# Performance work log

Measured on AMD Instinct MI355X. Metric: run time of the kernel, lower is better.

## Reference

```python
import jax, jax.numpy as jnp
import numpy as np

LR = 0.01
WD = 0.01


def _lfltm(params, x):
    w1, b1, w2, b2 = params
    return jnp.tanh(x @ w1 + b1) @ w2 + b2  # [N, D]


def _deep_opt_elem(Wm1, bm1, Wm2, bm2, g):
    # per-parameter-element learned optimizer: scalar grad -> hidden(M) -> scalar update
    h = jnp.tanh(g[..., None] * Wm1 + bm1)  # [..., M]
    return h @ Wm2 + bm2[0]


def setup_inputs() -> dict:
    key = jax.random.key(0)
    ks = jax.random.split(key, 8)
    N, D, H, M = 16384, 512, 1024, 32
    return {
        "x_t": jax.random.normal(ks[0], (N, D), jnp.float32),
        "x_target": jax.random.normal(ks[1], (N, D), jnp.float32),
        "w1": jax.random.normal(ks[2], (D, H), jnp.float32) * 0.02,
        "b1": jnp.zeros((H,), jnp.float32),
        "w2": jax.random.normal(ks[3], (H, D), jnp.float32) * 0.02,
        "b2": jnp.zeros((D,), jnp.float32),
        "Wm1": jax.random.normal(ks[4], (M,), jnp.float32) * 0.1,
        "bm1": jnp.zeros((M,), jnp.float32),
        "Wm2": jax.random.normal(ks[5], (M,), jnp.float32) * 0.1,
        "bm2": jnp.zeros((1,), jnp.float32),
    }


def reference(x_t, x_target, w1, b1, w2, b2, Wm1, bm1, Wm2, bm2):
    mem = (w1, b1, w2, b2)

    # retrieve: h_t = LFLTM(memory_state, x_t)
    h_t = _lfltm(mem, x_t)

    # analytic per-step gradient of MSE loss through the memory MLP
    def compute_loss(params):
        pred = _lfltm(params, x_t)
        return jnp.mean((pred - x_target) ** 2)

    grads = jax.grad(compute_loss)(mem)

    # learned optimizer on each gradient tensor, then fast-weight update
    new_mem = tuple(
        p - (LR * _deep_opt_elem(Wm1, bm1, Wm2, bm2, g) + WD * p)
        for p, g in zip(mem, grads)
    )

    return (h_t,) + new_mem
```

## Files before the change

kernel.cpp:

```cpp
#include <hip/hip_runtime.h>
#include <hip/hip_bf16.h>

#define LR 0.01f
#define WD 0.01f
#define NTHREADS 256
#define SCALE_G 1048576.0f
#define INV_SCALE_G 9.5367431640625e-07f

typedef short s16x8 __attribute__((ext_vector_type(8)));
typedef _Float16 f16x8 __attribute__((ext_vector_type(8)));
typedef float f32x4 __attribute__((ext_vector_type(4)));
typedef unsigned short u16;

__device__ __forceinline__ u16 f2h(float f) {
    _Float16 h = (_Float16)f;
    return *reinterpret_cast<u16*>(&h);
}
__device__ __forceinline__ float h2f(u16 u) {
    _Float16 h;
    *reinterpret_cast<u16*>(&h) = u;
    return (float)h;
}
__device__ __forceinline__ float tanh_fast(float x) {
    float t = fminf(fmaxf(2.f * x, -30.f), 30.f);
    float e = __expf(t);
    return 1.f - 2.f * __builtin_amdgcn_rcpf(e + 1.f);
}

__device__ __forceinline__ void stage_pair(const u16* gA, const u16* gB, int ldg,
                                           u16* lds) {
    const int t = threadIdx.x;
#pragma unroll
    for (int q = 0; q < 4; ++q) {
        int s = t + q * 256;
        int row = s >> 3, chp = s & 7;
        int chl = chp ^ (row & 7);
        const u16* gp = (chl < 4) ? (gA + (size_t)row * ldg + chl * 8)
                                  : (gB + (size_t)row * ldg + (chl & 3) * 8);
        __builtin_amdgcn_global_load_lds(
            (const __attribute__((address_space(1))) void*)gp,
            (__attribute__((address_space(3))) void*)(lds + s * 8), 16, 0, 0);
    }
}

__device__ __forceinline__ f16x8 frag(const u16* P, int r, int c) {
    return *(const f16x8*)(P + r * 64 + ((c ^ (r & 7)) * 8));
}

template <int EPI>
__global__ __launch_bounds__(NTHREADS) void k_mfma(
    const u16* __restrict__ A, const u16* __restrict__ Bt,
    int nbx, int Md, int Nd, int Kd, int Kslice,
    const float* __restrict__ bias, const float* __restrict__ xtgt,
    const u16* __restrict__ Th,
    float* __restrict__ outf, u16* __restrict__ outb, u16* __restrict__ outbT,
    float* __restrict__ gbias, float scale) {
    __shared__ u16 smem[2 * 8192];
    __shared__ float colacc[128];

    const int nwg = gridDim.x;
    const int sw = (blockIdx.x & 7) * (nwg >> 3) + (blockIdx.x >> 3);
    const int m0 = (sw / nbx) * 128, n0 = (sw % nbx) * 128;
    const int kb = blockIdx.y * Kslice;

    const int lane = threadIdx.x & 63, wid = threadIdx.x >> 6;
    const int wrow = (wid >> 1) * 64, wcol = (wid & 1) * 64;
    const int lm = lane & 15;
    const int cA = lane >> 4;

    f32x4 acc[4][4] = {};

    const u16* gA = A + (size_t)m0 * Kd + kb;
    const u16* gB = Bt + (size_t)n0 * Kd + kb;
    const int nt = Kslice >> 5;

    if (EPI == 1 || EPI == 2)
        if (threadIdx.x < 128) colacc[threadIdx.x] = 0.f;

    stage_pair(gA, gB, Kd, smem);
    stage_pair(gA + 32, gB + 32, Kd, smem + 8192);

    int cur = 0;
    for (int t = 0; t < nt; ++t, cur ^= 1) {
        if (t + 1 < nt) asm volatile("s_waitcnt vmcnt(4)" ::: "memory");
        else            asm volatile("s_waitcnt vmcnt(0)" ::: "memory");
        __builtin_amdgcn_s_barrier();

        const u16* P1 = smem + cur * 8192;
        f16x8 a[4], b[4];
#pragma unroll
        for (int i = 0; i < 4; ++i) {
            a[i] = frag(P1, wrow + i * 16 + lm, cA);
            b[i] = frag(P1, wcol + i * 16 + lm, cA + 4);
        }
        __builtin_amdgcn_s_setprio(1);
#pragma unroll
        for (int i = 0; i < 4; ++i)
#pragma unroll
            for (int j = 0; j < 4; ++j)
                acc[i][j] = __builtin_amdgcn_mfma_f32_16x16x32_f16(
                    a[i], b[j], acc[i][j], 0, 0, 0);
        __builtin_amdgcn_s_setprio(0);

        asm volatile("" ::: "memory");
        __builtin_amdgcn_s_barrier();
        if (t + 2 < nt)
            stage_pair(gA + (t + 2) * 32, gB + (t + 2) * 32, Kd,
                       smem + cur * 8192);
    }

    const int rbase = (lane >> 4) * 4;
#pragma unroll
    for (int i = 0; i < 4; ++i) {
        const int row0 = m0 + wrow + i * 16 + rbase;
#pragma unroll
        for (int j = 0; j < 4; ++j) {
            const int col = n0 + wcol + j * 16 + lm;
            if (EPI == 0) {
                ushort4 hv;
                float bcol = bias[col];
                hv.x = f2h(tanh_fast(acc[i][j][0] + bcol));
                hv.y = f2h(tanh_fast(acc[i][j][1] + bcol));
                hv.z = f2h(tanh_fast(acc[i][j][2] + bcol));
                hv.w = f2h(tanh_fast(acc[i][j][3] + bcol));
                outb[(size_t)(row0 + 0) * Nd + col] = hv.x;
                outb[(size_t)(row0 + 1) * Nd + col] = hv.y;
                outb[(size_t)(row0 + 2) * Nd + col] = hv.z;
                outb[(size_t)(row0 + 3) * Nd + col] = hv.w;
                *(ushort4*)(outbT + (size_t)col * Md + row0) = hv;
            } else if (EPI == 1) {
                ushort4 gv;
                float csum = 0.f;
#pragma unroll
                for (int r = 0; r < 4; ++r) {
                    size_t idx = (size_t)(row0 + r) * Nd + col;
                    float p = acc[i][j][r] + bias[col];
                    outf[idx] = p;
                    float gf = scale * (p - xtgt[idx]);
                    csum += gf;
                    u16 g = f2h(gf);
                    outb[idx] = g;
                    ((u16*)&gv)[r] = g;
                }
                *(ushort4*)(outbT + (size_t)col * Md + row0) = gv;
                atomicAdd(&colacc[wcol + j * 16 + lm], csum);
            } else if (EPI == 2) {
                ushort4 dv;
                float csum = 0.f;
#pragma unroll
                for (int r = 0; r < 4; ++r) {
                    size_t idx = (size_t)(row0 + r) * Nd + col;
                    float tv = h2f(Th[idx]);
                    float da = acc[i][j][r] * (1.0f - tv * tv);
                    csum += da;
                    ((u16*)&dv)[r] = f2h(da);
                }
                *(ushort4*)(outbT + (size_t)col * Md + row0) = dv;
                atomicAdd(&colacc[wcol + j * 16 + lm], csum);
            } else {
#pragma unroll
                for (int r = 0; r < 4; ++r)
                    atomicAdd(&outf[(size_t)(row0 + r) * Nd + col], acc[i][j][r]);
            }
        }
    }
    if (EPI == 1 || EPI == 2) {
        __syncthreads();
        if (threadIdx.x < 128)
            atomicAdd(&gbias[n0 + threadIdx.x], colacc[threadIdx.x]);
    }
}

__global__ void k_prep(const float* __restrict__ in, u16* __restrict__ rm,
                       u16* __restrict__ tr, int R, int C) {
    __shared__ float tile[64][65];
    const int tx = threadIdx.x & 63, ty = threadIdx.x >> 6;
    const int c0 = blockIdx.x * 64, r0 = blockIdx.y * 64;
#pragma unroll
    for (int i = 0; i < 64; i += 4) {
        size_t idx = (size_t)(r0 + ty + i) * C + c0 + tx;
        float v = in[idx];
        tile[ty + i][tx] = v;
        if (rm) rm[idx] = f2h(v);
    }
    __syncthreads();
    if (tr) {
#pragma unroll
        for (int i = 0; i < 64; i += 4)
            tr[(size_t)(c0 + ty + i) * R + r0 + tx] = f2h(tile[tx][ty + i]);
    }
}

__global__ void k_update_all(
    const float* __restrict__ w1, const float* __restrict__ b1,
    const float* __restrict__ w2, const float* __restrict__ b2,
    const float* __restrict__ g, float* __restrict__ out,
    int n1, int n2, int n3, int n4,
    const float* __restrict__ Wm1, const float* __restrict__ bm1,
    const float* __restrict__ Wm2, const float* __restrict__ bm2,
    int M, float invScale) {
    __shared__ float s1[64], s2[64], s3[64];
    if (threadIdx.x < M) {
        s1[threadIdx.x] = Wm1[threadIdx.x];
        s2[threadIdx.x] = bm1[threadIdx.x];
        s3[threadIdx.x] = Wm2[threadIdx.x];
    }
    __syncthreads();
    int i = blockIdx.x * blockDim.x + threadIdx.x;
    int n = n1 + n2 + n3 + n4;
    if (i >= n) return;
    const float* p;
    int off;
    if (i < n1) { p = w1; off = 0; }
    else if (i < n1 + n2) { p = b1; off = n1; }
    else if (i < n1 + n2 + n3) { p = w2; off = n1 + n2; }
    else { p = b2; off = n1 + n2 + n3; }
    float gv = g[i] * invScale;
    float u = bm2[0];
#pragma unroll 8
    for (int m = 0; m < M; ++m) u += tanh_fast(fmaf(gv, s1[m], s2[m])) * s3[m];
    float pv = p[i - off];
    out[i] = pv - (LR * u + WD * pv);
}

__global__ void k_zero(float* __restrict__ p, int n) {
    int i = blockIdx.x * blockDim.x + threadIdx.x;
    if (i < n) p[i] = 0.f;
}

extern "C" void kernel_launch(void* const* d_in, const int* in_sizes, int n_in,
                              void* d_out, int out_size, void* d_ws, size_t ws_size,
                              hipStream_t stream) {
    const float* x_t      = (const float*)d_in[0];
    const float* x_target = (const float*)d_in[1];
    const float* w1  = (const float*)d_in[2];
    const float* b1  = (const float*)d_in[3];
    const float* w2  = (const float*)d_in[4];
    const float* b2  = (const float*)d_in[5];
    const float* Wm1 = (const float*)d_in[6];
    const float* bm1 = (const float*)d_in[7];
    const float* Wm2 = (const float*)d_in[8];
    const float* bm2 = (const float*)d_in[9];

    const int H = in_sizes[3];
    const int D = in_sizes[5];
    const int N = in_sizes[0] / D;
    const int M = in_sizes[6];

    char* w = (char*)d_ws;
    float* gw1 = (float*)w;            w += (size_t)D * H * 4;
    float* gb1 = (float*)w;            w += (size_t)H * 4;
    float* gw2 = (float*)w;            w += (size_t)H * D * 4;
    float* gb2 = (float*)w;            w += (size_t)D * 4;
    u16* Tf   = (u16*)w;               w += (size_t)N * H * 2;
    u16* TT   = (u16*)w;               w += (size_t)N * H * 2;
    u16* dAT  = (u16*)w;               w += (size_t)N * H * 2;
    u16* Gb   = (u16*)w;               w += (size_t)N * D * 2;
    u16* GT   = (u16*)w;               w += (size_t)N * D * 2;
    u16* xf   = (u16*)w;               w += (size_t)N * D * 2;
    u16* xT   = (u16*)w;               w += (size_t)N * D * 2;
    u16* w1T  = (u16*)w;               w += (size_t)D * H * 2;
    u16* w2T  = (u16*)w;               w += (size_t)D * H * 2;
    u16* w2b  = (u16*)w;               w += (size_t)H * D * 2;

    float* out  = (float*)d_out;
    float* h_t  = out;
    float* o_w1 = h_t + (size_t)N * D;

    dim3 blk(NTHREADS);
    const float scaleG = (2.0f / ((float)N * (float)D)) * SCALE_G;

    int zn = D * H + H + H * D + D;
    k_zero<<<dim3((zn + NTHREADS - 1) / NTHREADS), blk, 0, stream>>>(gw1, zn);

    k_prep<<<dim3(D / 64, N / 64), blk, 0, stream>>>(x_t, xf, xT, N, D);
    k_prep<<<dim3(H / 64, D / 64), blk, 0, stream>>>(w1, nullptr, w1T, D, H);
    k_prep<<<dim3(D / 64, H / 64), blk, 0, stream>>>(w2, w2b, w2T, H, D);

    k_mfma<0><<<dim3((H / 128) * (N / 128), 1), blk, 0, stream>>>(
        xf, w1T, H / 128, N, H, D, D, b1, nullptr, nullptr,
        nullptr, Tf, TT, nullptr, 0.f);

    k_mfma<1><<<dim3((D / 128) * (N / 128), 1), blk, 0, stream>>>(
        Tf, w2T, D / 128, N, D, H, H, b2, x_target, nullptr,
        h_t, Gb, GT, gb2, scaleG);

    k_mfma<2><<<dim3((H / 128) * (N / 128), 1), blk, 0, stream>>>(
        Gb, w2b, H / 128, N, H, D, D, nullptr, nullptr, Tf,
        nullptr, nullptr, dAT, gb1, 0.f);

    const int SPLIT = 16;
    k_mfma<3><<<dim3((D / 128) * (H / 128), SPLIT), blk, 0, stream>>>(
        TT, GT, D / 128, H, D, N, N / SPLIT, nullptr, nullptr, nullptr,
        gw2, nullptr, nullptr, nullptr, 0.f);

    k_mfma<3><<<dim3((H / 128) * (D / 128), SPLIT), blk, 0, stream>>>(
        xT, dAT, H / 128, D, H, N, N / SPLIT, nullptr, nullptr, nullptr,
        gw1, nullptr, nullptr, nullptr, 0.f);

    int nAll = D * H + H + H * D + D;
    k_update_all<<<dim3((nAll + NTHREADS - 1) / NTHREADS), blk, 0, stream>>>(
        w1, b1, w2, b2, gw1, o_w1, D * H, H, H * D, D,
        Wm1, bm1, Wm2, bm2, M, INV_SCALE_G);
}
```

Before: 398.4 us.

## Stage epilogue outputs through LDS for coalesced stores; simplify K-loop pipelining

The epilogue now writes the f16 results into a padded LDS tile and then emits 16-byte coalesced stores for both the row-major and transposed outputs, replacing scattered 2-byte and 8-byte global stores. The main loop is also simplified from a two-ahead prefetch with fine-grained vmcnt waits and s_setprio to a one-ahead double buffer with a full __syncthreads each iteration. The coalesced stores are meant to cut wasted global memory transactions in the epilogue. The simpler loop may expose more load latency, and the extra barriers and LDS round trips add cost of their own.

```diff
diff --git a/kernel.cpp b/kernel.cpp
--- a/kernel.cpp
+++ b/kernel.cpp
@@ -6,6 +6,7 @@
 #define NTHREADS 256
 #define SCALE_G 1048576.0f
 #define INV_SCALE_G 9.5367431640625e-07f
+#define TRS 136
 
 typedef short s16x8 __attribute__((ext_vector_type(8)));
 typedef _Float16 f16x8 __attribute__((ext_vector_type(8)));
@@ -55,7 +56,7 @@
     const u16* __restrict__ Th,
     float* __restrict__ outf, u16* __restrict__ outb, u16* __restrict__ outbT,
     float* __restrict__ gbias, float scale) {
-    __shared__ u16 smem[2 * 8192];
+    __shared__ u16 smem[128 * TRS];
     __shared__ float colacc[128];
 
     const int nwg = gridDim.x;
@@ -72,20 +73,17 @@
 
     const u16* gA = A + (size_t)m0 * Kd + kb;
     const u16* gB = Bt + (size_t)n0 * Kd + kb;
-    const int nt = Kslice >> 5;
 
     if (EPI == 1 || EPI == 2)
         if (threadIdx.x < 128) colacc[threadIdx.x] = 0.f;
 
     stage_pair(gA, gB, Kd, smem);
-    stage_pair(gA + 32, gB + 32, Kd, smem + 8192);
+    __syncthreads();
 
     int cur = 0;
-    for (int t = 0; t < nt; ++t, cur ^= 1) {
-        if (t + 1 < nt) asm volatile("s_waitcnt vmcnt(4)" ::: "memory");
-        else            asm volatile("s_waitcnt vmcnt(0)" ::: "memory");
-        __builtin_amdgcn_s_barrier();
-
+    for (int k0 = 0; k0 < Kslice; k0 += 32, cur ^= 1) {
+        if (k0 + 32 < Kslice)
+            stage_pair(gA + k0 + 32, gB + k0 + 32, Kd, smem + (cur ^ 1) * 8192);
         const u16* P1 = smem + cur * 8192;
         f16x8 a[4], b[4];
 #pragma unroll
@@ -93,23 +91,33 @@
             a[i] = frag(P1, wrow + i * 16 + lm, cA);
             b[i] = frag(P1, wcol + i * 16 + lm, cA + 4);
         }
-        __builtin_amdgcn_s_setprio(1);
 #pragma unroll
         for (int i = 0; i < 4; ++i)
 #pragma unroll
             for (int j = 0; j < 4; ++j)
                 acc[i][j] = __builtin_amdgcn_mfma_f32_16x16x32_f16(
                     a[i], b[j], acc[i][j], 0, 0, 0);
-        __builtin_amdgcn_s_setprio(0);
-
-        asm volatile("" ::: "memory");
-        __builtin_amdgcn_s_barrier();
-        if (t + 2 < nt)
-            stage_pair(gA + (t + 2) * 32, gB + (t + 2) * 32, Kd,
-                       smem + cur * 8192);
+        __syncthreads();
     }
 
     const int rbase = (lane >> 4) * 4;
+
+    if (EPI == 3) {
+#pragma unroll
+        for (int i = 0; i < 4; ++i) {
+            const int row0 = m0 + wrow + i * 16 + rbase;
+#pragma unroll
+            for (int j = 0; j < 4; ++j) {
+                const int col = n0 + wcol + j * 16 + lm;
+#pragma unroll
+                for (int r = 0; r < 4; ++r)
+                    atomicAdd(&outf[(size_t)(row0 + r) * Nd + col], acc[i][j][r]);
+            }
+        }
+        return;
+    }
+
+    ushort4 hv[4][4];
 #pragma unroll
     for (int i = 0; i < 4; ++i) {
         const int row0 = m0 + wrow + i * 16 + rbase;
@@ -117,35 +125,25 @@
         for (int j = 0; j < 4; ++j) {
             const int col = n0 + wcol + j * 16 + lm;
             if (EPI == 0) {
-                ushort4 hv;
                 float bcol = bias[col];
-                hv.x = f2h(tanh_fast(acc[i][j][0] + bcol));
-                hv.y = f2h(tanh_fast(acc[i][j][1] + bcol));
-                hv.z = f2h(tanh_fast(acc[i][j][2] + bcol));
-                hv.w = f2h(tanh_fast(acc[i][j][3] + bcol));
-                outb[(size_t)(row0 + 0) * Nd + col] = hv.x;
-                outb[(size_t)(row0 + 1) * Nd + col] = hv.y;
-                outb[(size_t)(row0 + 2) * Nd + col] = hv.z;
-                outb[(size_t)(row0 + 3) * Nd + col] = hv.w;
-                *(ushort4*)(outbT + (size_t)col * Md + row0) = hv;
+                hv[i][j].x = f2h(tanh_fast(acc[i][j][0] + bcol));
+                hv[i][j].y = f2h(tanh_fast(acc[i][j][1] + bcol));
+                hv[i][j].z = f2h(tanh_fast(acc[i][j][2] + bcol));
+                hv[i][j].w = f2h(tanh_fast(acc[i][j][3] + bcol));
             } else if (EPI == 1) {
-                ushort4 gv;
                 float csum = 0.f;
+                float bcol = bias[col];
 #pragma unroll
                 for (int r = 0; r < 4; ++r) {
                     size_t idx = (size_t)(row0 + r) * Nd + col;
-                    float p = acc[i][j][r] + bias[col];
+                    float p = acc[i][j][r] + bcol;
                     outf[idx] = p;
                     float gf = scale * (p - xtgt[idx]);
                     csum += gf;
-                    u16 g = f2h(gf);
-                    outb[idx] = g;
-                    ((u16*)&gv)[r] = g;
+                    ((u16*)&hv[i][j])[r] = f2h(gf);
                 }
-                *(ushort4*)(outbT + (size_t)col * Md + row0) = gv;
                 atomicAdd(&colacc[wcol + j * 16 + lm], csum);
-            } else if (EPI == 2) {
-                ushort4 dv;
+            } else {
                 float csum = 0.f;
 #pragma unroll
                 for (int r = 0; r < 4; ++r) {
@@ -153,17 +151,48 @@
                     float tv = h2f(Th[idx]);
                     float da = acc[i][j][r] * (1.0f - tv * tv);
                     csum += da;
-                    ((u16*)&dv)[r] = f2h(da);
+                    ((u16*)&hv[i][j])[r] = f2h(da);
                 }
-                *(ushort4*)(outbT + (size_t)col * Md + row0) = dv;
                 atomicAdd(&colacc[wcol + j * 16 + lm], csum);
-            } else {
-#pragma unroll
-                for (int r = 0; r < 4; ++r)
-                    atomicAdd(&outf[(size_t)(row0 + r) * Nd + col], acc[i][j][r]);
             }
         }
     }
+
+#pragma unroll
+    for (int i = 0; i < 4; ++i)
+#pragma unroll
+        for (int j = 0; j < 4; ++j)
+            *(ushort4*)(smem + (wcol + j * 16 + lm) * TRS + (wrow + i * 16 + rbase)) =
+                hv[i][j];
+    __syncthreads();
+#pragma unroll
+    for (int p = 0; p < 8; ++p) {
+        int tr = wid * 32 + p * 4 + (lane >> 4);
+        int ch = lane & 15;
+        s16x8 v = *(const s16x8*)(smem + tr * TRS + ch * 8);
+        *(s16x8*)(outbT + (size_t)(n0 + tr) * Md + m0 + ch * 8) = v;
+    }
+
+    if (EPI <= 1) {
+        __syncthreads();
+#pragma unroll
+        for (int i = 0; i < 4; ++i)
+#pragma unroll
+            for (int j = 0; j < 4; ++j)
+#pragma unroll
+                for (int r = 0; r < 4; ++r)
+                    smem[(wrow + i * 16 + rbase + r) * TRS + wcol + j * 16 + lm] =
+                        ((u16*)&hv[i][j])[r];
+        __syncthreads();
+#pragma unroll
+        for (int p = 0; p < 8; ++p) {
+            int rr = wid * 32 + p * 4 + (lane >> 4);
+            int ch = lane & 15;
+            s16x8 v = *(const s16x8*)(smem + rr * TRS + ch * 8);
+            *(s16x8*)(outb + (size_t)(m0 + rr) * Nd + n0 + ch * 8) = v;
+        }
+    }
+
     if (EPI == 1 || EPI == 2) {
         __syncthreads();
         if (threadIdx.x < 128)
```

Result: faster. 380.8 us (-4.4%).
